# Kernel tuning notes

Measured on AMD Instinct MI355X. Metric: run time of the kernel, lower is better.

## Reference

```python
import jax, jax.numpy as jnp
import numpy as np

MARGIN = 1.0
EPS = 1e-6  # torch F.pairwise_distance eps


def setup_inputs() -> dict:
    key = jax.random.key(0)
    k1, k2, k3, k4, k5 = jax.random.split(key, 5)
    B, C, H, W = 128, 1024, 14, 14
    return {
        "feat": jax.random.normal(k1, (B, C, H, W), dtype=jnp.float32),
        "feat_p": jax.random.normal(k2, (B, C, H, W), dtype=jnp.float32),
        "avg_feat": jax.random.normal(k3, (2, C, 1, 1), dtype=jnp.float32),
        "qual": jax.random.randint(k4, (B,), 0, 2, dtype=jnp.int64),
        "label": jax.random.randint(k5, (B,), 0, 2, dtype=jnp.int64),
    }


def reference(feat, feat_p, avg_feat, qual, label):
    # AdaptiveAvgPool2d(1): global average over H, W -> [B, C]
    f = feat.mean(axis=(2, 3))
    fp = feat_p.mean(axis=(2, 3))
    # torch code concatenates f[qual==1] and fp[qual==0]; since qual is binary
    # this is a permutation of per-sample selections and the final sum is
    # permutation-invariant, so select per-sample instead of gathering.
    sel = jnp.where((qual == 1)[:, None], f, fp)  # [B, C] anchors
    af = avg_feat[:, :, 0, 0]  # [2, C]
    pos = af[label]            # [B, C]
    neg = af[1 - label]        # [B, C]
    # TripletMarginLoss on [C,1,1] tensors: pairwise_distance reduces the last
    # dim (size 1) with p=2, i.e. d = |a - b + eps| elementwise; then mean
    # over the C*1 elements, summed over the batch.
    d_ap = jnp.abs(sel - pos + EPS)
    d_an = jnp.abs(sel - neg + EPS)
    per_sample = jnp.maximum(d_ap - d_an + MARGIN, 0.0).mean(axis=1)  # [B]
    return per_sample.sum()
```

## Files before the change

kernel.cpp:

```cpp
#include <hip/hip_runtime.h>


#define B_ 128
#define C_ 1024
#define HW_ 196
#define NF4_ 49
#define TPB_ 256
#define NBLOCKS_ (B_ * C_ / TPB_)

__global__ __launch_bounds__(TPB_) void loss_partial_kernel(
    const float* __restrict__ feat, const float* __restrict__ feat_p,
    const float* __restrict__ af, const int* __restrict__ qual,
    const int* __restrict__ label, float* __restrict__ ws)
{
    const int blk = blockIdx.x;
    const int b   = blk >> 2;
    const int c   = ((blk & 3) << 8) | threadIdx.x;

    const int q   = qual[b];
    const int lab = label[b];
    const float* sel = (q == 1 ? feat : feat_p);
    const float4* p = (const float4*)(sel + ((size_t)b * C_ + c) * HW_);

    float s0 = 0.f, s1 = 0.f, s2 = 0.f, s3 = 0.f;
    #pragma unroll
    for (int i = 0; i < NF4_; ++i) {
        float4 v = p[i];
        s0 += v.x; s1 += v.y; s2 += v.z; s3 += v.w;
    }
    const float mean = ((s0 + s1) + (s2 + s3)) * (1.0f / 196.0f);

    const float pos = af[lab * C_ + c];
    const float neg = af[(1 - lab) * C_ + c];
    const float dap = fabsf(mean - pos + 1e-6f);
    const float dan = fabsf(mean - neg + 1e-6f);
    float h = fmaxf(dap - dan + 1.0f, 0.0f);

    #pragma unroll
    for (int off = 32; off > 0; off >>= 1)
        h += __shfl_xor(h, off, 64);
    __shared__ float sred[TPB_ / 64];
    const int wave = threadIdx.x >> 6;
    if ((threadIdx.x & 63) == 0) sred[wave] = h;
    __syncthreads();
    if (threadIdx.x == 0)
        ws[blk] = (sred[0] + sred[1]) + (sred[2] + sred[3]);
}

__global__ __launch_bounds__(TPB_) void final_reduce_kernel(
    const float* __restrict__ ws, float* __restrict__ out)
{
    const int tid = threadIdx.x;
    float s = ws[tid] + ws[tid + TPB_];
    #pragma unroll
    for (int off = 32; off > 0; off >>= 1)
        s += __shfl_xor(s, off, 64);
    __shared__ float sred[TPB_ / 64];
    if ((tid & 63) == 0) sred[tid >> 6] = s;
    __syncthreads();
    if (tid == 0)
        out[0] = ((sred[0] + sred[1]) + (sred[2] + sred[3])) * (1.0f / (float)C_);
}

extern "C" void kernel_launch(void* const* d_in, const int* in_sizes, int n_in,
                              void* d_out, int out_size, void* d_ws, size_t ws_size,
                              hipStream_t stream) {
    const float* feat   = (const float*)d_in[0];
    const float* feat_p = (const float*)d_in[1];
    const float* af     = (const float*)d_in[2];
    const int*   qual   = (const int*)d_in[3];
    const int*   label  = (const int*)d_in[4];
    float* out = (float*)d_out;
    float* ws  = (float*)d_ws;

    loss_partial_kernel<<<NBLOCKS_, TPB_, 0, stream>>>(feat, feat_p, af, qual, label, ws);
    final_reduce_kernel<<<1, TPB_, 0, stream>>>(ws, out);
}
```

Before: 218.7 us.

## Coalesce feature loads across a wave and reduce per-channel sums through LDS

```diff
diff --git a/kernel.cpp b/kernel.cpp
--- a/kernel.cpp
+++ b/kernel.cpp
@@ -5,57 +5,72 @@
 #define C_ 1024
 #define HW_ 196
 #define NF4_ 49
-#define TPB_ 256
-#define NBLOCKS_ (B_ * C_ / TPB_)
+#define CPB_ 64
+#define NBLOCKS_ (B_ * C_ / CPB_)
+#define LDSN_ (CPB_ * NF4_)
 
-__global__ __launch_bounds__(TPB_) void loss_partial_kernel(
+__global__ __launch_bounds__(64) void loss_partial_kernel(
     const float* __restrict__ feat, const float* __restrict__ feat_p,
     const float* __restrict__ af, const int* __restrict__ qual,
     const int* __restrict__ label, float* __restrict__ ws)
 {
-    const int blk = blockIdx.x;
-    const int b   = blk >> 2;
-    const int c   = ((blk & 3) << 8) | threadIdx.x;
+    __shared__ float lsum[LDSN_];
+    const int blk  = blockIdx.x;
+    const int b    = blk >> 4;
+    const int cg   = blk & 15;
+    const int lane = threadIdx.x;
+    const int c0   = cg << 6;
 
     const int q   = qual[b];
     const int lab = label[b];
     const float* sel = (q == 1 ? feat : feat_p);
-    const float4* p = (const float4*)(sel + ((size_t)b * C_ + c) * HW_);
+    const float4* base = (const float4*)(sel + ((size_t)b * C_ + c0) * HW_);
 
-    float s0 = 0.f, s1 = 0.f, s2 = 0.f, s3 = 0.f;
     #pragma unroll
-    for (int i = 0; i < NF4_; ++i) {
-        float4 v = p[i];
-        s0 += v.x; s1 += v.y; s2 += v.z; s3 += v.w;
+    for (int chunk = 0; chunk < 7; ++chunk) {
+        float4 t[7];
+        #pragma unroll
+        for (int k = 0; k < 7; ++k)
+            t[k] = base[(chunk * 7 + k) * 64 + lane];
+        #pragma unroll
+        for (int k = 0; k < 7; ++k)
+            lsum[(chunk * 7 + k) * 64 + lane] =
+                (t[k].x + t[k].y) + (t[k].z + t[k].w);
     }
-    const float mean = ((s0 + s1) + (s2 + s3)) * (1.0f / 196.0f);
+    __syncthreads();
 
+    const float* my = &lsum[lane * NF4_];
+    float a0 = 0.f, a1 = 0.f, a2 = 0.f, a3 = 0.f;
+    #pragma unroll
+    for (int j = 0; j < 48; j += 4) {
+        a0 += my[j]; a1 += my[j + 1]; a2 += my[j + 2]; a3 += my[j + 3];
+    }
+    const float s = ((a0 + a1) + (a2 + a3)) + my[48];
+    const float mean = s * (1.0f / 196.0f);
+
+    const int c = c0 + lane;
     const float pos = af[lab * C_ + c];
     const float neg = af[(1 - lab) * C_ + c];
-    const float dap = fabsf(mean - pos + 1e-6f);
-    const float dan = fabsf(mean - neg + 1e-6f);
-    float h = fmaxf(dap - dan + 1.0f, 0.0f);
+    float h = fmaxf(fabsf(mean - pos + 1e-6f) - fabsf(mean - neg + 1e-6f) + 1.0f, 0.0f);
 
     #pragma unroll
     for (int off = 32; off > 0; off >>= 1)
         h += __shfl_xor(h, off, 64);
-    __shared__ float sred[TPB_ / 64];
-    const int wave = threadIdx.x >> 6;
-    if ((threadIdx.x & 63) == 0) sred[wave] = h;
-    __syncthreads();
-    if (threadIdx.x == 0)
-        ws[blk] = (sred[0] + sred[1]) + (sred[2] + sred[3]);
+    if (lane == 0) ws[blk] = h;
 }
 
-__global__ __launch_bounds__(TPB_) void final_reduce_kernel(
+__global__ __launch_bounds__(256) void final_reduce_kernel(
     const float* __restrict__ ws, float* __restrict__ out)
 {
     const int tid = threadIdx.x;
-    float s = ws[tid] + ws[tid + TPB_];
+    float s = 0.0f;
+    #pragma unroll
+    for (int i = 0; i < NBLOCKS_ / 256; ++i)
+        s += ws[tid + i * 256];
     #pragma unroll
     for (int off = 32; off > 0; off >>= 1)
         s += __shfl_xor(s, off, 64);
-    __shared__ float sred[TPB_ / 64];
+    __shared__ float sred[4];
     if ((tid & 63) == 0) sred[tid >> 6] = s;
     __syncthreads();
     if (tid == 0)
@@ -73,6 +88,6 @@
     float* out = (float*)d_out;
     float* ws  = (float*)d_ws;
 
-    loss_partial_kernel<<<NBLOCKS_, TPB_, 0, stream>>>(feat, feat_p, af, qual, label, ws);
-    final_reduce_kernel<<<1, TPB_, 0, stream>>>(ws, out);
+    loss_partial_kernel<<<NBLOCKS_, 64, 0, stream>>>(feat, feat_p, af, qual, label, ws);
+    final_reduce_kernel<<<1, 256, 0, stream>>>(ws, out);
 }
```

New measurement: 199.9 us. 1.09x faster.
